# Kernel optimization log

Measured on AMD Instinct MI355X. Metric: run time of the kernel, lower is better.

The kernel has to match this reference:

```python
import jax, jax.numpy as jnp
import numpy as np

B, S, H = 4, 1024, 1024
R = 512          # num_rules
M = 1024         # memory_size
HEADS = 16
STEPS = 3        # inference_steps
TEMP = 1.0       # softmax_temperature
LN_EPS = 1e-5


def setup_inputs() -> dict:
    key = jax.random.key(0)
    ks = jax.random.split(key, 40)
    std = 0.02
    p = lambda k, shp: (jax.random.normal(k, shp, jnp.float32) * std)
    inp = {
        "hidden_states": jax.random.normal(ks[0], (B, S, H), jnp.float32),
        "rule_embeddings": p(ks[1], (R, H)),
        "rule_sel_w": p(ks[2], (H, R)), "rule_sel_b": jnp.zeros((R,), jnp.float32),
        # self-attention (nn.MultiheadAttention) projections
        "attn_wq": p(ks[3], (H, H)), "attn_bq": jnp.zeros((H,), jnp.float32),
        "attn_wk": p(ks[4], (H, H)), "attn_bk": jnp.zeros((H,), jnp.float32),
        "attn_wv": p(ks[5], (H, H)), "attn_bv": jnp.zeros((H,), jnp.float32),
        "attn_wo": p(ks[6], (H, H)), "attn_bo": jnp.zeros((H,), jnp.float32),
        # memory bank + key/query/value projections
        "memory": p(ks[7], (M, H)),
        "mem_q_w": p(ks[8], (H, H)), "mem_q_b": jnp.zeros((H,), jnp.float32),
        "mem_k_w": p(ks[9], (H, H)), "mem_k_b": jnp.zeros((H,), jnp.float32),
        "mem_v_w": p(ks[10], (H, H)), "mem_v_b": jnp.zeros((H,), jnp.float32),
        # memory_attention (nn.MultiheadAttention) projections
        "mattn_wq": p(ks[11], (H, H)), "mattn_bq": jnp.zeros((H,), jnp.float32),
        "mattn_wk": p(ks[12], (H, H)), "mattn_bk": jnp.zeros((H,), jnp.float32),
        "mattn_wv": p(ks[13], (H, H)), "mattn_bv": jnp.zeros((H,), jnp.float32),
        "mattn_wo": p(ks[14], (H, H)), "mattn_bo": jnp.zeros((H,), jnp.float32),
        # rule_application: Linear(2H,H)+LN+GELU+Linear(H,H)
        "ra_w1": p(ks[15], (2 * H, H)), "ra_b1": jnp.zeros((H,), jnp.float32),
        "ra_ln_s": jnp.ones((H,), jnp.float32), "ra_ln_b": jnp.zeros((H,), jnp.float32),
        "ra_w2": p(ks[16], (H, H)), "ra_b2": jnp.zeros((H,), jnp.float32),
        # confidence_scorer
        "conf_w": p(ks[17], (H, 1)), "conf_b": jnp.zeros((1,), jnp.float32),
    }
    return inp


def _mha(q_in, k_in, v_in, wq, bq, wk, bk, wv, bv, wo, bo):
    # standard nn.MultiheadAttention math (batch_first, eval mode -> no dropout)
    b, sq, h = q_in.shape
    d = h // HEADS
    qh = (q_in @ wq + bq).reshape(b, sq, HEADS, d)
    kh = (k_in @ wk + bk).reshape(b, -1, HEADS, d)
    vh = (v_in @ wv + bv).reshape(b, -1, HEADS, d)
    scores = jnp.einsum('bqhd,bkhd->bhqk', qh, kh) / jnp.sqrt(jnp.asarray(d, qh.dtype))
    probs = jax.nn.softmax(scores, axis=-1)
    out = jnp.einsum('bhqk,bkhd->bqhd', probs, vh).reshape(b, sq, h)
    return out @ wo + bo


def _ln(x, s, b):
    mu = x.mean(-1, keepdims=True)
    var = ((x - mu) ** 2).mean(-1, keepdims=True)
    return (x - mu) / jnp.sqrt(var + LN_EPS) * s + b


def reference(hidden_states, rule_embeddings, rule_sel_w, rule_sel_b,
              attn_wq, attn_bq, attn_wk, attn_bk, attn_wv, attn_bv, attn_wo, attn_bo,
              memory, mem_q_w, mem_q_b, mem_k_w, mem_k_b, mem_v_w, mem_v_b,
              mattn_wq, mattn_bq, mattn_wk, mattn_bk, mattn_wv, mattn_bv, mattn_wo, mattn_bo,
              ra_w1, ra_b1, ra_ln_s, ra_ln_b, ra_w2, ra_b2, conf_w, conf_b):
    h = hidden_states
    b = h.shape[0]
    # memory keys/values are input-independent: project once, broadcast over batch
    mk = jnp.broadcast_to((memory @ mem_k_w + mem_k_b)[None], (b, M, H))
    mv = jnp.broadcast_to((memory @ mem_v_w + mem_v_b)[None], (b, M, H))
    for _ in range(STEPS):
        # rule routing: soft selection over the rule-embedding table
        rule_probs = jax.nn.softmax((h @ rule_sel_w + rule_sel_b) / TEMP, axis=-1)  # [B,S,R]
        selected = jnp.einsum('bsr,rh->bsh', rule_probs, rule_embeddings)           # [B,S,H]
        # self-attention reasoning
        h = h + _mha(h, h, h, attn_wq, attn_bq, attn_wk, attn_bk,
                     attn_wv, attn_bv, attn_wo, attn_bo)
        # memory attention
        mq = h @ mem_q_w + mem_q_b
        h = h + _mha(mq, mk, mv, mattn_wq, mattn_bq, mattn_wk, mattn_bk,
                     mattn_wv, mattn_bv, mattn_wo, mattn_bo)
        # rule application MLP on [h ; selected_rules]
        x = jnp.concatenate([h, selected], axis=-1)                                  # [B,S,2H]
        u = jax.nn.gelu(_ln(x @ ra_w1 + ra_b1, ra_ln_s, ra_ln_b), approximate=False)
        h = h + (u @ ra_w2 + ra_b2)
    confidence = jax.nn.sigmoid(h @ conf_w + conf_b)  # [B,S,1]
    return h, confidence
```

## Files before the change

kernel.cpp:

```cpp
#include <hip/hip_runtime.h>
#include <stdint.h>

typedef _Float16 f16;
typedef __attribute__((ext_vector_type(4))) float floatx4;
typedef __attribute__((ext_vector_type(8))) f16   f16x8;
typedef __attribute__((ext_vector_type(4))) f16   f16x4;

#define GLD_LDS16(gp, lp)                                                                      \
  __builtin_amdgcn_global_load_lds((const __attribute__((address_space(1))) void*)(uintptr_t)(gp), \
                                   (__attribute__((address_space(3))) void*)(uintptr_t)(lp), 16, 0, 0)

struct SrlOut {
  int n0;
  const float* bias;
  const float* resid;
  float* Cf; f16* Cb;
  int ldcf, ldcb, transV;
  long long sCb, sCh;
};
struct SrlGemmArgs {
  const f16* A; const f16* B;
  int M, N, K, lda, ldb;
  long long sAb, sAh, sBb, sBh;
  float alpha;
  int nOuts;
  SrlOut out[4];
};

template<int BN>
__global__ __launch_bounds__(256, 2) void srl_gemm(SrlGemmArgs g) {
  constexpr int BM = 128, BK = 64;
  constexpr int BCH = BN / 32;
  constexpr int MI  = (BN == 128) ? 4 : 2;
  __shared__ f16 As[2][BM * BK];
  __shared__ f16 Bs[2][BN * BK];
  const int tid  = threadIdx.x;
  const int wid  = tid >> 6;
  const int lane = tid & 63;
  const int z  = blockIdx.z, zh = z & 15, zb = z >> 4;

  const int gx = gridDim.x;
  const int NT = gx * gridDim.y;
  const int L  = blockIdx.y * gx + blockIdx.x;
  const int W  = ((NT & 7) == 0) ? ((L & 7) * (NT >> 3) + (L >> 3)) : L;
  const int tn = (W % gx) * BN;
  const int tm = (W / gx) * BM;

  const f16* Ab = g.A + (long long)zb * g.sAb + (long long)zh * g.sAh + (long long)tm * g.lda;
  const f16* Bb = g.B + (long long)zb * g.sBb + (long long)zh * g.sBh + (long long)tn * g.ldb;
  const int maxAr = g.M - 1 - tm;
  const int maxBr = g.N - 1 - tn;

  int aR[4], aO[4];
#pragma unroll
  for (int i = 0; i < 4; ++i) {
    int e = wid * 2048 + i * 512 + lane * 8;
    int r = e >> 6, s = (e >> 3) & 7;
    aR[i] = r; aO[i] = ((s - r) & 7) * 8;
  }
  int bR[BCH], bO[BCH];
#pragma unroll
  for (int i = 0; i < BCH; ++i) {
    int e = wid * (BN * 16) + i * 512 + lane * 8;
    int r = e >> 6, s = (e >> 3) & 7;
    bR[i] = r; bO[i] = ((s - r) & 7) * 8;
  }

  f16x8 pa[4], pb[BCH];
  auto loadT = [&](int k0) {
#pragma unroll
    for (int i = 0; i < 4; ++i) {
      int r = aR[i] <= maxAr ? aR[i] : maxAr;
      pa[i] = *(const f16x8*)(Ab + (long long)r * g.lda + (k0 + aO[i]));
    }
#pragma unroll
    for (int i = 0; i < BCH; ++i) {
      int r = bR[i] <= maxBr ? bR[i] : maxBr;
      pb[i] = *(const f16x8*)(Bb + (long long)r * g.ldb + (k0 + bO[i]));
    }
  };
  auto storeT = [&](int buf) {
    f16* a = As[buf] + wid * 2048 + lane * 8;
    f16* b = Bs[buf] + wid * (BN * 16) + lane * 8;
#pragma unroll
    for (int i = 0; i < 4; ++i) *(f16x8*)(a + i * 512) = pa[i];
#pragma unroll
    for (int i = 0; i < BCH; ++i) *(f16x8*)(b + i * 512) = pb[i];
  };

  floatx4 acc[MI][4];
#pragma unroll
  for (int a = 0; a < MI; ++a)
#pragma unroll
    for (int b = 0; b < 4; ++b) {
      acc[a][b][0] = 0.f; acc[a][b][1] = 0.f; acc[a][b][2] = 0.f; acc[a][b][3] = 0.f;
    }

  const int wm = (BN == 128) ? (wid & 1) * 64 : wid * 32;
  const int wn = (BN == 128) ? (wid >> 1) * 64 : 0;
  const int lm = lane & 15;
  const int quad = lane >> 4;

  const int T = g.K / BK;
  loadT(0);
  storeT(0);
  if (T > 1) loadT(BK);
  __syncthreads();

  for (int t = 0; t < T; ++t) {
    const int cb = t & 1;
    if (t + 1 < T) {
      storeT(cb ^ 1);
      if (t + 2 < T) loadT((t + 2) * BK);
    }
#pragma unroll
    for (int ks = 0; ks < 2; ++ks) {
      f16x8 af[MI], bfr[4];
#pragma unroll
      for (int mi = 0; mi < MI; ++mi) {
        int row = wm + mi * 16 + lm;
        int sg = ((ks * 4 + quad) + row) & 7;
        af[mi] = *(const f16x8*)(As[cb] + row * 64 + sg * 8);
      }
#pragma unroll
      for (int ni = 0; ni < 4; ++ni) {
        int row = wn + ni * 16 + lm;
        int sg = ((ks * 4 + quad) + row) & 7;
        bfr[ni] = *(const f16x8*)(Bs[cb] + row * 64 + sg * 8);
      }
#pragma unroll
      for (int mi = 0; mi < MI; ++mi)
#pragma unroll
        for (int ni = 0; ni < 4; ++ni)
          acc[mi][ni] = __builtin_amdgcn_mfma_f32_16x16x32_f16(af[mi], bfr[ni], acc[mi][ni], 0, 0, 0);
    }
    __syncthreads();
  }

  int oi = 0;
  for (int j = 1; j < g.nOuts; ++j)
    if (tn >= g.out[j].n0) oi = j;
  const SrlOut O = g.out[oi];
  const long long zc = (long long)zb * O.sCb + (long long)zh * O.sCh;
#pragma unroll
  for (int mi = 0; mi < MI; ++mi) {
#pragma unroll
    for (int r = 0; r < 4; ++r) {
      int m = tm + wm + mi * 16 + quad * 4 + r;
      if (m >= g.M) continue;
#pragma unroll
      for (int ni = 0; ni < 4; ++ni) {
        int n = tn + wn + ni * 16 + lm;
        if (n >= g.N) continue;
        int nl = n - O.n0;
        float v = acc[mi][ni][r] * g.alpha;
        if (O.bias)  v += O.bias[nl];
        if (O.resid) v += O.resid[(long long)m * O.ldcf + nl];
        if (O.Cf)    O.Cf[zc + (long long)m * O.ldcf + nl] = v;
        if (O.Cb) {
          long long idx = O.transV
              ? ((long long)(m >> 10) * 1048576 + (long long)nl * 1024 + (m & 1023))
              : (zc + (long long)m * O.ldcb + nl);
          O.Cb[idx] = (f16)v;
        }
      }
    }
  }
}

struct SrlFlashArgs {
  const f16* Q; const f16* K; const f16* VT; f16* O;
  long long sQb, sKb, sVb;
  float scale;
};

__global__ __launch_bounds__(256, 2) void srl_flash(SrlFlashArgs a) {
  __shared__ f16 Qs[8192];
  __shared__ f16 Ks[8192];
  __shared__ f16 VTs[8192];
  __shared__ f16 Ps[4][4096];
  const int tid = threadIdx.x, wid = tid >> 6, lane = tid & 63;
  const int quad = lane >> 4, c = lane & 15;
  const int L = blockIdx.x;
  const int bh = (L & 7) + ((L >> 6) << 3);
  const int qt = (L >> 3) & 7;
  const int b = bh >> 4, h = bh & 15;
  const f16* Qg = a.Q + (long long)b * a.sQb + (long long)qt * 131072 + h * 64;
  const f16* Kg = a.K + (long long)b * a.sKb + h * 64;
  const f16* Vg = a.VT + (long long)b * a.sVb + (long long)h * 65536;
  f16* Og = a.O + (long long)b * 1048576 + (long long)qt * 131072 + h * 64;

  int rRow[4], rOff[4];
#pragma unroll
  for (int i = 0; i < 4; ++i) {
    int e = wid * 2048 + i * 512 + lane * 8;
    int r = e >> 6, gL = (e >> 3) & 7;
    rRow[i] = r; rOff[i] = ((gL - r) & 7) * 8;
  }
  int vRow[4], vOff[4];
#pragma unroll
  for (int i = 0; i < 4; ++i) {
    int e = wid * 2048 + i * 512 + lane * 8;
    int d = e >> 7, gL = (e >> 3) & 15;
    vRow[i] = d; vOff[i] = ((gL - (d & 7)) & 15) * 8;
  }

#pragma unroll
  for (int i = 0; i < 4; ++i)
    GLD_LDS16(Qg + (long long)rRow[i] * 1024 + rOff[i], Qs + wid * 2048 + i * 512);
  __syncthreads();

  const int wq = wid * 32;
  f16x8 qf[2][2];
#pragma unroll
  for (int nf = 0; nf < 2; ++nf)
#pragma unroll
    for (int ch = 0; ch < 2; ++ch) {
      int row = wq + nf * 16 + c;
      int slot = ((ch * 4 + quad) + row) & 7;
      f16x8 v = *(const f16x8*)(Qs + row * 64 + slot * 8);
      f16 sc = (f16)a.scale;
#pragma unroll
      for (int j = 0; j < 8; ++j) v[j] = v[j] * sc;
      qf[nf][ch] = v;
    }

  float l_s[2] = {0.f, 0.f};
  floatx4 Oa[2][4];
#pragma unroll
  for (int nf = 0; nf < 2; ++nf)
#pragma unroll
    for (int no = 0; no < 4; ++no) {
      Oa[nf][no][0] = 0.f; Oa[nf][no][1] = 0.f; Oa[nf][no][2] = 0.f; Oa[nf][no][3] = 0.f;
    }

  for (int t = 0; t < 8; ++t) {
    __syncthreads();
#pragma unroll
    for (int i = 0; i < 4; ++i)
      GLD_LDS16(Kg + (long long)(t * 128 + rRow[i]) * 1024 + rOff[i], Ks + wid * 2048 + i * 512);
#pragma unroll
    for (int i = 0; i < 4; ++i)
      GLD_LDS16(Vg + (long long)vRow[i] * 1024 + (t * 128 + vOff[i]), VTs + wid * 2048 + i * 512);
    __syncthreads();

    floatx4 sT[2][8];
#pragma unroll
    for (int nf = 0; nf < 2; ++nf)
#pragma unroll
      for (int mf = 0; mf < 8; ++mf) {
        sT[nf][mf][0] = 0.f; sT[nf][mf][1] = 0.f; sT[nf][mf][2] = 0.f; sT[nf][mf][3] = 0.f;
      }
#pragma unroll
    for (int ch = 0; ch < 2; ++ch)
#pragma unroll
      for (int mf = 0; mf < 8; ++mf) {
        int key = mf * 16 + c;
        int slot = ((ch * 4 + quad) + key) & 7;
        f16x8 kf = *(const f16x8*)(Ks + key * 64 + slot * 8);
        sT[0][mf] = __builtin_amdgcn_mfma_f32_16x16x32_f16(kf, qf[0][ch], sT[0][mf], 0, 0, 0);
        sT[1][mf] = __builtin_amdgcn_mfma_f32_16x16x32_f16(kf, qf[1][ch], sT[1][mf], 0, 0, 0);
      }

#pragma unroll
    for (int nf = 0; nf < 2; ++nf) {
      float lt = 0.f;
      const int q = nf * 16 + c;
#pragma unroll
      for (int mf = 0; mf < 8; ++mf) {
        f16x4 pk;
#pragma unroll
        for (int r = 0; r < 4; ++r) {
          float p = __builtin_amdgcn_exp2f(sT[nf][mf][r]);
          lt += p;
          pk[r] = (f16)p;
        }
        int kg = mf * 2 + (quad >> 1), sub = (quad & 1) * 4;
        int slot = (kg + (q & 7)) & 15;
        *(f16x4*)(Ps[wid] + q * 128 + slot * 8 + sub) = pk;
      }
      lt += __shfl_xor(lt, 16);
      lt += __shfl_xor(lt, 32);
      l_s[nf] += lt;
    }
#pragma unroll
    for (int cc = 0; cc < 4; ++cc) {
      f16x8 af[2];
#pragma unroll
      for (int nf = 0; nf < 2; ++nf) {
        int q = nf * 16 + c;
        int slot = ((cc * 4 + quad) + (q & 7)) & 15;
        af[nf] = *(const f16x8*)(Ps[wid] + q * 128 + slot * 8);
      }
#pragma unroll
      for (int no = 0; no < 4; ++no) {
        int d = no * 16 + c;
        int slot = ((cc * 4 + quad) + (d & 7)) & 15;
        f16x8 vf = *(const f16x8*)(VTs + d * 128 + slot * 8);
        Oa[0][no] = __builtin_amdgcn_mfma_f32_16x16x32_f16(af[0], vf, Oa[0][no], 0, 0, 0);
        Oa[1][no] = __builtin_amdgcn_mfma_f32_16x16x32_f16(af[1], vf, Oa[1][no], 0, 0, 0);
      }
    }
  }

#pragma unroll
  for (int nf = 0; nf < 2; ++nf)
#pragma unroll
    for (int r = 0; r < 4; ++r) {
      float li = 1.f / __shfl(l_s[nf], quad * 4 + r);
      int qrow = wq + nf * 16 + quad * 4 + r;
#pragma unroll
      for (int no = 0; no < 4; ++no)
        Qs[qrow * 64 + no * 16 + c] = (f16)(Oa[nf][no][r] * li);
    }
  __syncthreads();
#pragma unroll
  for (int i = 0; i < 4; ++i) {
    int e = wid * 2048 + i * 512 + lane * 8;
    int row = e >> 6, col = e & 63;
    *(f16x8*)(Og + (long long)row * 1024 + col) = *(const f16x8*)(Qs + e);
  }
}

__global__ __launch_bounds__(256) void srl_softmax_rule(const float* logits, f16* probs) {
  __shared__ float red[16];
  const long long row = blockIdx.x;
  const float* p = logits + row * 512;
  const int tid = threadIdx.x;
  float v0 = p[tid], v1 = p[tid + 256];
  float mx = fmaxf(v0, v1);
#pragma unroll
  for (int o = 32; o > 0; o >>= 1) mx = fmaxf(mx, __shfl_down(mx, o));
  const int wid = tid >> 6, lane = tid & 63;
  if (lane == 0) red[wid] = mx;
  __syncthreads();
  if (tid == 0) red[8] = fmaxf(fmaxf(red[0], red[1]), fmaxf(red[2], red[3]));
  __syncthreads();
  mx = red[8];
  float e0 = __expf(v0 - mx), e1 = __expf(v1 - mx);
  float s = e0 + e1;
#pragma unroll
  for (int o = 32; o > 0; o >>= 1) s += __shfl_down(s, o);
  if (lane == 0) red[wid + 4] = s;
  __syncthreads();
  if (tid == 0) red[9] = 1.f / (red[4] + red[5] + red[6] + red[7]);
  __syncthreads();
  const float inv = red[9];
  probs[row * 512 + tid] = (f16)(e0 * inv);
  probs[row * 512 + tid + 256] = (f16)(e1 * inv);
}

__global__ __launch_bounds__(256) void srl_ln_gelu(const float* x, const float* gam, const float* bet, f16* out) {
  __shared__ float red[16];
  const long long row = blockIdx.x;
  const float* p = x + row * 1024;
  const int tid = threadIdx.x;
  float4 xv = *(const float4*)(p + tid * 4);
  float v[4] = {xv.x, xv.y, xv.z, xv.w};
  float s = v[0] + v[1] + v[2] + v[3];
  float s2 = v[0] * v[0] + v[1] * v[1] + v[2] * v[2] + v[3] * v[3];
#pragma unroll
  for (int o = 32; o > 0; o >>= 1) { s += __shfl_down(s, o); s2 += __shfl_down(s2, o); }
  const int wid = tid >> 6, lane = tid & 63;
  if (lane == 0) { red[wid] = s; red[wid + 4] = s2; }
  __syncthreads();
  if (tid == 0) {
    float ts = red[0] + red[1] + red[2] + red[3];
    float ts2 = red[4] + red[5] + red[6] + red[7];
    float mu = ts * (1.f / 1024.f);
    float var = ts2 * (1.f / 1024.f) - mu * mu;
    red[8] = mu;
    red[9] = rsqrtf(var + 1e-5f);
  }
  __syncthreads();
  const float mu = red[8], rstd = red[9];
  f16x4 o4;
#pragma unroll
  for (int i = 0; i < 4; ++i) {
    int c = tid * 4 + i;
    float t = (v[i] - mu) * rstd * gam[c] + bet[c];
    float ge = 0.5f * t * (1.f + erff(t * 0.70710678118654752f));
    o4[i] = (f16)ge;
  }
  *(f16x4*)(out + row * 1024 + tid * 4) = o4;
}

struct SrlTcEnt { const float* src; f16* dst; int rows, cols, trans, tileStart; };
struct SrlTcArgs { SrlTcEnt e[16]; };

__global__ __launch_bounds__(256) void srl_convert_weights(SrlTcArgs a) {
  __shared__ float t[32][33];
  const int bt = blockIdx.x;
  int ei = 0;
#pragma unroll
  for (int j = 1; j < 16; ++j)
    if (bt >= a.e[j].tileStart) ei = j;
  SrlTcEnt E = a.e[ei];
  const int lt = bt - E.tileStart;
  const int tcols = E.cols >> 5;
  const int tr = lt / tcols;
  const int tc = lt - tr * tcols;
  const int r = threadIdx.x >> 5;
  const int c = threadIdx.x & 31;
  if (!E.trans) {
#pragma unroll
    for (int p = 0; p < 4; ++p) {
      long long rr = tr * 32 + r + p * 8;
      long long idx = rr * E.cols + tc * 32 + c;
      E.dst[idx] = (f16)E.src[idx];
    }
  } else {
#pragma unroll
    for (int p = 0; p < 4; ++p)
      t[r + p * 8][c] = E.src[(long long)(tr * 32 + r + p * 8) * E.cols + tc * 32 + c];
    __syncthreads();
#pragma unroll
    for (int p = 0; p < 4; ++p)
      E.dst[(long long)(tc * 32 + r + p * 8) * E.rows + tr * 32 + c] = (f16)t[c][r + p * 8];
  }
}

__global__ __launch_bounds__(256) void srl_prep_bias(const float* rsel_b, const float* bq,
                                                     const float* bk, const float* bv,
                                                     const float* bmq, const float* maq_w,
                                                     const float* bmaq,
                                                     float* bias_qkvr, float* bcomp) {
  int i = blockIdx.x * 256 + threadIdx.x;
  if (i < 3584) {
    float v;
    if (i < 512) v = rsel_b[i];
    else if (i < 1536) v = bq[i - 512];
    else if (i < 2560) v = bk[i - 1536];
    else v = bv[i - 2560];
    bias_qkvr[i] = v;
  } else if (i < 3584 + 1024) {
    int m = i - 3584;
    float s = bmaq[m];
    for (int t = 0; t < 1024; ++t) s += bmq[t] * maq_w[(long long)t * 1024 + m];
    bcomp[m] = s;
  }
}

__global__ __launch_bounds__(256) void srl_h_init(const float* hidden, float* hf, f16* hx) {
  long long base = ((long long)blockIdx.x * 256 + threadIdx.x) * 4;
  float4 v = *(const float4*)(hidden + base);
  *(float4*)(hf + base) = v;
  long long row = base >> 10;
  int col = (int)(base & 1023);
  f16x4 b;
  b[0] = (f16)v.x; b[1] = (f16)v.y; b[2] = (f16)v.z; b[3] = (f16)v.w;
  *(f16x4*)(hx + row * 2048 + col) = b;
}

__global__ __launch_bounds__(256) void srl_finalize(const float* hf, const float* w, const float* b,
                                                    float* out, float* conf) {
  const int bid = blockIdx.x;
  if (bid < 4096) {
    long long base = ((long long)bid * 256 + threadIdx.x) * 4;
    *(float4*)(out + base) = *(const float4*)(hf + base);
  } else {
    const int row = (bid - 4096) * 4 + (threadIdx.x >> 6);
    const int lane = threadIdx.x & 63;
    const float* p = hf + (long long)row * 1024;
    float s = 0.f;
    for (int j = lane; j < 1024; j += 64) s += p[j] * w[j];
#pragma unroll
    for (int o = 32; o > 0; o >>= 1) s += __shfl_down(s, o);
    if (lane == 0) conf[row] = 1.f / (1.f + __expf(-(s + b[0])));
  }
}

extern "C" void kernel_launch(void* const* d_in, const int* in_sizes, int n_in,
                              void* d_out, int out_size, void* d_ws, size_t ws_size,
                              hipStream_t stream) {
  (void)in_sizes; (void)n_in; (void)out_size; (void)ws_size;
  const float* in_hidden   = (const float*)d_in[0];
  const float* in_rule_emb = (const float*)d_in[1];
  const float* in_rsel_w   = (const float*)d_in[2];
  const float* in_rsel_b   = (const float*)d_in[3];
  const float* in_attn_wq  = (const float*)d_in[4];
  const float* in_attn_bq  = (const float*)d_in[5];
  const float* in_attn_wk  = (const float*)d_in[6];
  const float* in_attn_bk  = (const float*)d_in[7];
  const float* in_attn_wv  = (const float*)d_in[8];
  const float* in_attn_bv  = (const float*)d_in[9];
  const float* in_attn_wo  = (const float*)d_in[10];
  const float* in_attn_bo  = (const float*)d_in[11];
  const float* in_memory   = (const float*)d_in[12];
  const float* in_mq_w     = (const float*)d_in[13];
  const float* in_mq_b     = (const float*)d_in[14];
  const float* in_mk_w     = (const float*)d_in[15];
  const float* in_mk_b     = (const float*)d_in[16];
  const float* in_mv_w     = (const float*)d_in[17];
  const float* in_mv_b     = (const float*)d_in[18];
  const float* in_maq_w    = (const float*)d_in[19];
  const float* in_maq_b    = (const float*)d_in[20];
  const float* in_mak_w    = (const float*)d_in[21];
  const float* in_mak_b    = (const float*)d_in[22];
  const float* in_mav_w    = (const float*)d_in[23];
  const float* in_mav_b    = (const float*)d_in[24];
  const float* in_mao_w    = (const float*)d_in[25];
  const float* in_mao_b    = (const float*)d_in[26];
  const float* in_ra_w1    = (const float*)d_in[27];
  const float* in_ra_b1    = (const float*)d_in[28];
  const float* in_ln_s     = (const float*)d_in[29];
  const float* in_ln_b     = (const float*)d_in[30];
  const float* in_ra_w2    = (const float*)d_in[31];
  const float* in_ra_b2    = (const float*)d_in[32];
  const float* in_conf_w   = (const float*)d_in[33];
  const float* in_conf_b   = (const float*)d_in[34];

  char* ws = (char*)d_ws;
  size_t off = 0;
  auto alloc = [&](size_t bytes) -> void* {
    void* p = ws + off;
    off = (off + bytes + 255) & ~(size_t)255;
    return p;
  };
  f16* wt_qkvr    = (f16*)alloc(3584 * 1024 * 2);
  float* bias_qkvr= (float*)alloc(3584 * 4);
  f16* wt_attn_o  = (f16*)alloc(1048576 * 2);
  f16* wt_mq_comp = (f16*)alloc(1048576 * 2);
  float* bcomp    = (float*)alloc(1024 * 4);
  f16* wt_mattn_o = (f16*)alloc(1048576 * 2);
  f16* wt_ra1     = (f16*)alloc(2097152 * 2);
  f16* wt_ra2     = (f16*)alloc(1048576 * 2);
  f16* wt_remb    = (f16*)alloc(524288 * 2);
  f16* wt_mem_kv  = (f16*)alloc(2097152 * 2);
  f16* wt_mattn_k = (f16*)alloc(1048576 * 2);
  f16* wt_mattn_v = (f16*)alloc(1048576 * 2);
  f16* mem_h      = (f16*)alloc(1048576 * 2);
  f16* mk_h       = (f16*)alloc(1048576 * 2);
  f16* mv_h       = (f16*)alloc(1048576 * 2);
  f16* mak_h      = (f16*)alloc(1048576 * 2);
  f16* mavT_h     = (f16*)alloc(1048576 * 2);
  float* h_f      = (float*)alloc(4194304 * 4);
  f16* hx         = (f16*)alloc(8388608 * 2);
  f16* q_h        = (f16*)alloc(4194304 * 2);
  f16* k_h        = (f16*)alloc(4194304 * 2);
  f16* vT_h       = (f16*)alloc(4194304 * 2);
  f16* ctx_h      = (f16*)alloc(4194304 * 2);
  f16* u_h        = (f16*)alloc(4194304 * 2);
  char* arena     = (char*)alloc(16777216);
  float* logits_f = (float*)arena;
  f16* probs_h    = (f16*)(arena + 8388608);
  float* ra1_f    = (float*)arena;
  f16* mqw_nt     = (f16*)arena;
  f16* wmaq_t     = (f16*)(arena + 2097152);

  auto mkOut = [](int n0, const float* bias, const float* resid, float* Cf, int ldcf,
                  f16* Cb, int ldcb, int transV, long long sCb, long long sCh) {
    SrlOut o;
    o.n0 = n0; o.bias = bias; o.resid = resid; o.Cf = Cf; o.Cb = Cb;
    o.ldcf = ldcf; o.ldcb = ldcb; o.transV = transV; o.sCb = sCb; o.sCh = sCh;
    return o;
  };
  auto run = [&](int BN, int M, int N, int K, const f16* A, int lda, const f16* B, int ldb,
                 float alpha, int Z, long long sAb, long long sAh, long long sBb, long long sBh,
                 SrlGemmArgs g) {
    g.A = A; g.B = B; g.M = M; g.N = N; g.K = K; g.lda = lda; g.ldb = ldb;
    g.sAb = sAb; g.sAh = sAh; g.sBb = sBb; g.sBh = sBh; g.alpha = alpha;
    dim3 grid((N + BN - 1) / BN, (M + 127) / 128, Z);
    if (BN == 128) hipLaunchKernelGGL(srl_gemm<128>, grid, dim3(256), 0, stream, g);
    else           hipLaunchKernelGGL(srl_gemm<64>,  grid, dim3(256), 0, stream, g);
  };
  auto run1 = [&](int BN, int M, int N, int K, const f16* A, int lda, const f16* B, int ldb,
                  float alpha, const float* bias, const float* resid, float* Cf, int ldcf,
                  f16* Cb, int ldcb, int transV) {
    SrlGemmArgs g{};
    g.nOuts = 1;
    g.out[0] = mkOut(0, bias, resid, Cf, ldcf, Cb, ldcb, transV, 0, 0);
    run(BN, M, N, K, A, lda, B, ldb, alpha, 1, 0, 0, 0, 0, g);
  };

  SrlTcArgs tc;
  int ts = 0;
  auto setent = [&](int i, const float* s, f16* d, int rows, int cols, int trans) {
    tc.e[i].src = s; tc.e[i].dst = d; tc.e[i].rows = rows; tc.e[i].cols = cols;
    tc.e[i].trans = trans; tc.e[i].tileStart = ts;
    ts += (rows / 32) * (cols / 32);
  };
  setent(0,  in_attn_wq, wt_qkvr + 512 * 1024, 1024, 1024, 1);
  setent(1,  in_attn_wk, wt_qkvr + 1536 * 1024, 1024, 1024, 1);
  setent(2,  in_attn_wv, wt_qkvr + 2560 * 1024, 1024, 1024, 1);
  setent(3,  in_rsel_w,  wt_qkvr, 1024, 512, 1);
  setent(4,  in_attn_wo, wt_attn_o, 1024, 1024, 1);
  setent(5,  in_mq_w,    mqw_nt, 1024, 1024, 0);
  setent(6,  in_maq_w,   wmaq_t, 1024, 1024, 1);
  setent(7,  in_mak_w,   wt_mattn_k, 1024, 1024, 1);
  setent(8,  in_mav_w,   wt_mattn_v, 1024, 1024, 1);
  setent(9,  in_mk_w,    wt_mem_kv, 1024, 1024, 1);
  setent(10, in_mv_w,    wt_mem_kv + 1048576, 1024, 1024, 1);
  setent(11, in_mao_w,   wt_mattn_o, 1024, 1024, 1);
  setent(12, in_ra_w1,   wt_ra1, 2048, 1024, 1);
  setent(13, in_ra_w2,   wt_ra2, 1024, 1024, 1);
  setent(14, in_rule_emb, wt_remb, 512, 1024, 1);
  setent(15, in_memory,  mem_h, 1024, 1024, 0);
  hipLaunchKernelGGL(srl_convert_weights, dim3(ts), dim3(256), 0, stream, tc);
  hipLaunchKernelGGL(srl_prep_bias, dim3(18), dim3(256), 0, stream,
                     in_rsel_b, in_attn_bq, in_attn_bk, in_attn_bv,
                     in_mq_b, in_maq_w, in_maq_b, bias_qkvr, bcomp);
  hipLaunchKernelGGL(srl_h_init, dim3(4096), dim3(256), 0, stream, in_hidden, h_f, hx);

  {
    SrlGemmArgs g{};
    g.nOuts = 2;
    g.out[0] = mkOut(0, in_mk_b, nullptr, nullptr, 0, mk_h, 1024, 0, 0, 0);
    g.out[1] = mkOut(1024, in_mv_b, nullptr, nullptr, 0, mv_h, 1024, 0, 0, 0);
    run(64, 1024, 2048, 1024, mem_h, 1024, wt_mem_kv, 1024, 1.f, 1, 0, 0, 0, 0, g);
  }
  run1(64, 1024, 1024, 1024, mk_h, 1024, wt_mattn_k, 1024, 1.f, in_mak_b, nullptr, nullptr, 0, mak_h, 1024, 0);
  run1(64, 1024, 1024, 1024, mv_h, 1024, wt_mattn_v, 1024, 1.f, in_mav_b, nullptr, nullptr, 0, mavT_h, 0, 1);
  run1(64, 1024, 1024, 1024, wmaq_t, 1024, mqw_nt, 1024, 1.f, nullptr, nullptr, nullptr, 0, wt_mq_comp, 1024, 0);

  const float kLog2e = 1.4426950408889634f;
  for (int step = 0; step < 3; ++step) {
    {
      SrlGemmArgs g{};
      g.nOuts = 4;
      g.out[0] = mkOut(0,    bias_qkvr,        nullptr, logits_f, 512, nullptr, 0, 0, 0, 0);
      g.out[1] = mkOut(512,  bias_qkvr + 512,  nullptr, nullptr, 0, q_h, 1024, 0, 0, 0);
      g.out[2] = mkOut(1536, bias_qkvr + 1536, nullptr, nullptr, 0, k_h, 1024, 0, 0, 0);
      g.out[3] = mkOut(2560, bias_qkvr + 2560, nullptr, nullptr, 0, vT_h, 0, 1, 0, 0);
      run(128, 4096, 3584, 1024, hx, 2048, wt_qkvr, 1024, 1.f, 1, 0, 0, 0, 0, g);
    }
    hipLaunchKernelGGL(srl_softmax_rule, dim3(4096), dim3(256), 0, stream, logits_f, probs_h);
    run1(64, 4096, 1024, 512, probs_h, 512, wt_remb, 512, 1.f, nullptr, nullptr, nullptr, 0, hx + 1024, 2048, 0);
    {
      SrlFlashArgs fa;
      fa.Q = q_h; fa.K = k_h; fa.VT = vT_h; fa.O = ctx_h;
      fa.sQb = 1048576; fa.sKb = 1048576; fa.sVb = 1048576; fa.scale = 0.125f * kLog2e;
      hipLaunchKernelGGL(srl_flash, dim3(512), dim3(256), 0, stream, fa);
    }
    run1(64, 4096, 1024, 1024, ctx_h, 1024, wt_attn_o, 1024, 1.f, in_attn_bo, h_f, h_f, 1024, hx, 2048, 0);
    run1(64, 4096, 1024, 1024, hx, 2048, wt_mq_comp, 1024, 1.f, bcomp, nullptr, nullptr, 0, k_h, 1024, 0);
    {
      SrlFlashArgs fa;
      fa.Q = k_h; fa.K = mak_h; fa.VT = mavT_h; fa.O = ctx_h;
      fa.sQb = 1048576; fa.sKb = 0; fa.sVb = 0; fa.scale = 0.125f * kLog2e;
      hipLaunchKernelGGL(srl_flash, dim3(512), dim3(256), 0, stream, fa);
    }
    run1(64, 4096, 1024, 1024, ctx_h, 1024, wt_mattn_o, 1024, 1.f, in_mao_b, h_f, h_f, 1024, hx, 2048, 0);
    run1(64, 4096, 1024, 2048, hx, 2048, wt_ra1, 2048, 1.f, in_ra_b1, nullptr, ra1_f, 1024, nullptr, 0, 0);
    hipLaunchKernelGGL(srl_ln_gelu, dim3(4096), dim3(256), 0, stream, ra1_f, in_ln_s, in_ln_b, u_h);
    run1(64, 4096, 1024, 1024, u_h, 1024, wt_ra2, 1024, 1.f, in_ra_b2, h_f, h_f, 1024, hx, 2048, 0);
  }

  hipLaunchKernelGGL(srl_finalize, dim3(5120), dim3(256), 0, stream, h_f, in_conf_w, in_conf_b,
                     (float*)d_out, (float*)d_out + 4194304);
}
```

Measured before the change: 1.241 ms.

## Add single-buffer 128x64 direct-to-LDS GEMM for QKVR and split-K the ra1 GEMM

Adds srl_gemm2, a 2-wave 128x64 tile kernel that loads A and B straight into LDS through global_load_lds with a single buffer. The fused QKV+rule GEMM now uses it in place of the 128x128 register-staged kernel. The K=2048 rule-application GEMM is split into two K=1024 halves via the z grid dimension, each writing its own fp32 partial. The LayerNorm+GELU kernel then sums both partials and the bias. The aim is more blocks in flight for better occupancy, at the cost of an extra 16MB fp32 partial write and read, and a single LDS buffer with no prefetch in the new kernel.

```diff
diff --git a/kernel.cpp b/kernel.cpp
--- a/kernel.cpp
+++ b/kernel.cpp
@@ -27,11 +27,8 @@
   SrlOut out[4];
 };
 
-template<int BN>
-__global__ __launch_bounds__(256, 2) void srl_gemm(SrlGemmArgs g) {
-  constexpr int BM = 128, BK = 64;
-  constexpr int BCH = BN / 32;
-  constexpr int MI  = (BN == 128) ? 4 : 2;
+__global__ __launch_bounds__(256, 2) void srl_gemm_db(SrlGemmArgs g) {
+  constexpr int BN = 64, BM = 128, BK = 64, BCH = 2, MI = 2;
   __shared__ f16 As[2][BM * BK];
   __shared__ f16 Bs[2][BN * BK];
   const int tid  = threadIdx.x;
@@ -96,8 +93,7 @@
       acc[a][b][0] = 0.f; acc[a][b][1] = 0.f; acc[a][b][2] = 0.f; acc[a][b][3] = 0.f;
     }
 
-  const int wm = (BN == 128) ? (wid & 1) * 64 : wid * 32;
-  const int wn = (BN == 128) ? (wid >> 1) * 64 : 0;
+  const int wm = wid * 32;
   const int lm = lane & 15;
   const int quad = lane >> 4;
 
@@ -124,7 +120,7 @@
       }
 #pragma unroll
       for (int ni = 0; ni < 4; ++ni) {
-        int row = wn + ni * 16 + lm;
+        int row = ni * 16 + lm;
         int sg = ((ks * 4 + quad) + row) & 7;
         bfr[ni] = *(const f16x8*)(Bs[cb] + row * 64 + sg * 8);
       }
@@ -150,7 +146,124 @@
       if (m >= g.M) continue;
 #pragma unroll
       for (int ni = 0; ni < 4; ++ni) {
-        int n = tn + wn + ni * 16 + lm;
+        int n = tn + ni * 16 + lm;
+        if (n >= g.N) continue;
+        int nl = n - O.n0;
+        float v = acc[mi][ni][r] * g.alpha;
+        if (O.bias)  v += O.bias[nl];
+        if (O.resid) v += O.resid[(long long)m * O.ldcf + nl];
+        if (O.Cf)    O.Cf[zc + (long long)m * O.ldcf + nl] = v;
+        if (O.Cb) {
+          long long idx = O.transV
+              ? ((long long)(m >> 10) * 1048576 + (long long)nl * 1024 + (m & 1023))
+              : (zc + (long long)m * O.ldcb + nl);
+          O.Cb[idx] = (f16)v;
+        }
+      }
+    }
+  }
+}
+
+__global__ __launch_bounds__(128, 2) void srl_gemm2(SrlGemmArgs g) {
+  constexpr int BK = 64;
+  __shared__ f16 As[128 * BK];
+  __shared__ f16 Bs[64 * BK];
+  const int tid  = threadIdx.x;
+  const int wid  = tid >> 6;
+  const int lane = tid & 63;
+  const int z  = blockIdx.z, zh = z & 15, zb = z >> 4;
+
+  const int gx = gridDim.x;
+  const int NT = gx * gridDim.y;
+  const int L  = blockIdx.y * gx + blockIdx.x;
+  const int W  = ((NT & 7) == 0) ? ((L & 7) * (NT >> 3) + (L >> 3)) : L;
+  const int tn = (W % gx) * 64;
+  const int tm = (W / gx) * 128;
+
+  const f16* Ab = g.A + (long long)zb * g.sAb + (long long)zh * g.sAh + (long long)tm * g.lda;
+  const f16* Bb = g.B + (long long)zb * g.sBb + (long long)zh * g.sBh + (long long)tn * g.ldb;
+  const int maxAr = g.M - 1 - tm;
+  const int maxBr = g.N - 1 - tn;
+
+  int aR[8], aO[8];
+#pragma unroll
+  for (int i = 0; i < 8; ++i) {
+    int e = wid * 4096 + i * 512 + lane * 8;
+    int r = e >> 6, s = (e >> 3) & 7;
+    aR[i] = r; aO[i] = ((s - r) & 7) * 8;
+  }
+  int bR[4], bO[4];
+#pragma unroll
+  for (int i = 0; i < 4; ++i) {
+    int e = wid * 2048 + i * 512 + lane * 8;
+    int r = e >> 6, s = (e >> 3) & 7;
+    bR[i] = r; bO[i] = ((s - r) & 7) * 8;
+  }
+  f16* lA = As + wid * 4096;
+  f16* lB = Bs + wid * 2048;
+
+  floatx4 acc[4][4];
+#pragma unroll
+  for (int a = 0; a < 4; ++a)
+#pragma unroll
+    for (int b = 0; b < 4; ++b) {
+      acc[a][b][0] = 0.f; acc[a][b][1] = 0.f; acc[a][b][2] = 0.f; acc[a][b][3] = 0.f;
+    }
+
+  const int wm = wid * 64;
+  const int lm = lane & 15;
+  const int quad = lane >> 4;
+
+  for (int k0 = 0; k0 < g.K; k0 += BK) {
+    __syncthreads();
+#pragma unroll
+    for (int i = 0; i < 8; ++i) {
+      int r = aR[i] <= maxAr ? aR[i] : maxAr;
+      GLD_LDS16(Ab + (long long)r * g.lda + (k0 + aO[i]), lA + i * 512);
+    }
+#pragma unroll
+    for (int i = 0; i < 4; ++i) {
+      int r = bR[i] <= maxBr ? bR[i] : maxBr;
+      GLD_LDS16(Bb + (long long)r * g.ldb + (k0 + bO[i]), lB + i * 512);
+    }
+    __syncthreads();
+#pragma unroll
+    for (int ks = 0; ks < 2; ++ks) {
+      f16x8 af[4], bfr[4];
+#pragma unroll
+      for (int mi = 0; mi < 4; ++mi) {
+        int row = wm + mi * 16 + lm;
+        int sg = ((ks * 4 + quad) + row) & 7;
+        af[mi] = *(const f16x8*)(As + row * 64 + sg * 8);
+      }
+#pragma unroll
+      for (int ni = 0; ni < 4; ++ni) {
+        int row = ni * 16 + lm;
+        int sg = ((ks * 4 + quad) + row) & 7;
+        bfr[ni] = *(const f16x8*)(Bs + row * 64 + sg * 8);
+      }
+#pragma unroll
+      for (int mi = 0; mi < 4; ++mi)
+#pragma unroll
+        for (int ni = 0; ni < 4; ++ni)
+          acc[mi][ni] = __builtin_amdgcn_mfma_f32_16x16x32_f16(af[mi], bfr[ni], acc[mi][ni], 0, 0, 0);
+    }
+  }
+
+  int oi = 0;
+  for (int j = 1; j < g.nOuts; ++j)
+    if (tn >= g.out[j].n0) oi = j;
+  const SrlOut O = g.out[oi];
+  const long long zc = (long long)zb * O.sCb + (long long)zh * O.sCh;
+#pragma unroll
+  for (int mi = 0; mi < 4; ++mi) {
+#pragma unroll
+    for (int r = 0; r < 4; ++r) {
+      int m = tm + wm + mi * 16 + quad * 4 + r;
+      if (m >= g.M) continue;
+#pragma unroll
+      for (int ni = 0; ni < 4; ++ni) {
+        int n = tn + ni * 16 + lm;
         if (n >= g.N) continue;
         int nl = n - O.n0;
         float v = acc[mi][ni][r] * g.alpha;
@@ -350,13 +463,16 @@
   probs[row * 512 + tid + 256] = (f16)(e1 * inv);
 }
 
-__global__ __launch_bounds__(256) void srl_ln_gelu(const float* x, const float* gam, const float* bet, f16* out) {
+__global__ __launch_bounds__(256) void srl_ln_gelu2(const float* x0, const float* x1,
+                                                    const float* b1,
+                                                    const float* gam, const float* bet, f16* out) {
   __shared__ float red[16];
   const long long row = blockIdx.x;
-  const float* p = x + row * 1024;
   const int tid = threadIdx.x;
-  float4 xv = *(const float4*)(p + tid * 4);
-  float v[4] = {xv.x, xv.y, xv.z, xv.w};
+  float4 a0 = *(const float4*)(x0 + row * 1024 + tid * 4);
+  float4 a1 = *(const float4*)(x1 + row * 1024 + tid * 4);
+  float4 bb = *(const float4*)(b1 + tid * 4);
+  float v[4] = {a0.x + a1.x + bb.x, a0.y + a1.y + bb.y, a0.z + a1.z + bb.z, a0.w + a1.w + bb.w};
   float s = v[0] + v[1] + v[2] + v[3];
   float s2 = v[0] * v[0] + v[1] * v[1] + v[2] * v[2] + v[3] * v[3];
 #pragma unroll
@@ -541,10 +657,11 @@
   f16* vT_h       = (f16*)alloc(4194304 * 2);
   f16* ctx_h      = (f16*)alloc(4194304 * 2);
   f16* u_h        = (f16*)alloc(4194304 * 2);
-  char* arena     = (char*)alloc(16777216);
+  char* arena     = (char*)alloc(33554432);
   float* logits_f = (float*)arena;
   f16* probs_h    = (f16*)(arena + 8388608);
-  float* ra1_f    = (float*)arena;
+  float* ra1_p0   = (float*)arena;
+  float* ra1_p1   = (float*)(arena + 16777216);
   f16* mqw_nt     = (f16*)arena;
   f16* wmaq_t     = (f16*)(arena + 2097152);
 
@@ -555,22 +672,28 @@
     o.ldcf = ldcf; o.ldcb = ldcb; o.transV = transV; o.sCb = sCb; o.sCh = sCh;
     return o;
   };
-  auto run = [&](int BN, int M, int N, int K, const f16* A, int lda, const f16* B, int ldb,
-                 float alpha, int Z, long long sAb, long long sAh, long long sBb, long long sBh,
-                 SrlGemmArgs g) {
+  auto runDb = [&](int M, int N, int K, const f16* A, int lda, const f16* B, int ldb,
+                   float alpha, int Z, long long sAb, long long sAh, long long sBb, long long sBh,
+                   SrlGemmArgs g) {
     g.A = A; g.B = B; g.M = M; g.N = N; g.K = K; g.lda = lda; g.ldb = ldb;
     g.sAb = sAb; g.sAh = sAh; g.sBb = sBb; g.sBh = sBh; g.alpha = alpha;
-    dim3 grid((N + BN - 1) / BN, (M + 127) / 128, Z);
-    if (BN == 128) hipLaunchKernelGGL(srl_gemm<128>, grid, dim3(256), 0, stream, g);
-    else           hipLaunchKernelGGL(srl_gemm<64>,  grid, dim3(256), 0, stream, g);
+    dim3 grid((N + 63) / 64, (M + 127) / 128, Z);
+    hipLaunchKernelGGL(srl_gemm_db, grid, dim3(256), 0, stream, g);
   };
-  auto run1 = [&](int BN, int M, int N, int K, const f16* A, int lda, const f16* B, int ldb,
-                  float alpha, const float* bias, const float* resid, float* Cf, int ldcf,
-                  f16* Cb, int ldcb, int transV) {
+  auto runDb1 = [&](int M, int N, int K, const f16* A, int lda, const f16* B, int ldb,
+                    float alpha, const float* bias, const float* resid, float* Cf, int ldcf,
+                    f16* Cb, int ldcb, int transV) {
     SrlGemmArgs g{};
     g.nOuts = 1;
     g.out[0] = mkOut(0, bias, resid, Cf, ldcf, Cb, ldcb, transV, 0, 0);
-    run(BN, M, N, K, A, lda, B, ldb, alpha, 1, 0, 0, 0, 0, g);
+    runDb(M, N, K, A, lda, B, ldb, alpha, 1, 0, 0, 0, 0, g);
+  };
+  auto runW2 = [&](int M, int N, int K, const f16* A, int lda, const f16* B, int ldb,
+                   float alpha, SrlGemmArgs g) {
+    g.A = A; g.B = B; g.M = M; g.N = N; g.K = K; g.lda = lda; g.ldb = ldb;
+    g.sAb = 0; g.sAh = 0; g.sBb = 0; g.sBh = 0; g.alpha = alpha;
+    dim3 grid((N + 63) / 64, (M + 127) / 128, 1);
+    hipLaunchKernelGGL(srl_gemm2, grid, dim3(128), 0, stream, g);
   };
 
   SrlTcArgs tc;
@@ -607,11 +730,11 @@
     g.nOuts = 2;
     g.out[0] = mkOut(0, in_mk_b, nullptr, nullptr, 0, mk_h, 1024, 0, 0, 0);
     g.out[1] = mkOut(1024, in_mv_b, nullptr, nullptr, 0, mv_h, 1024, 0, 0, 0);
-    run(64, 1024, 2048, 1024, mem_h, 1024, wt_mem_kv, 1024, 1.f, 1, 0, 0, 0, 0, g);
-  }
-  run1(64, 1024, 1024, 1024, mk_h, 1024, wt_mattn_k, 1024, 1.f, in_mak_b, nullptr, nullptr, 0, mak_h, 1024, 0);
-  run1(64, 1024, 1024, 1024, mv_h, 1024, wt_mattn_v, 1024, 1.f, in_mav_b, nullptr, nullptr, 0, mavT_h, 0, 1);
-  run1(64, 1024, 1024, 1024, wmaq_t, 1024, mqw_nt, 1024, 1.f, nullptr, nullptr, nullptr, 0, wt_mq_comp, 1024, 0);
+    runDb(1024, 2048, 1024, mem_h, 1024, wt_mem_kv, 1024, 1.f, 1, 0, 0, 0, 0, g);
+  }
+  runDb1(1024, 1024, 1024, mk_h, 1024, wt_mattn_k, 1024, 1.f, in_mak_b, nullptr, nullptr, 0, mak_h, 1024, 0);
+  runDb1(1024, 1024, 1024, mv_h, 1024, wt_mattn_v, 1024, 1.f, in_mav_b, nullptr, nullptr, 0, mavT_h, 0, 1);
+  runDb1(1024, 1024, 1024, wmaq_t, 1024, mqw_nt, 1024, 1.f, nullptr, nullptr, nullptr, 0, wt_mq_comp, 1024, 0);
 
   const float kLog2e = 1.4426950408889634f;
   for (int step = 0; step < 3; ++step) {
@@ -622,28 +745,34 @@
       g.out[1] = mkOut(512,  bias_qkvr + 512,  nullptr, nullptr, 0, q_h, 1024, 0, 0, 0);
       g.out[2] = mkOut(1536, bias_qkvr + 1536, nullptr, nullptr, 0, k_h, 1024, 0, 0, 0);
       g.out[3] = mkOut(2560, bias_qkvr + 2560, nullptr, nullptr, 0, vT_h, 0, 1, 0, 0);
-      run(128, 4096, 3584, 1024, hx, 2048, wt_qkvr, 1024, 1.f, 1, 0, 0, 0, 0, g);
+      runW2(4096, 3584, 1024, hx, 2048, wt_qkvr, 1024, 1.f, g);
     }
     hipLaunchKernelGGL(srl_softmax_rule, dim3(4096), dim3(256), 0, stream, logits_f, probs_h);
-    run1(64, 4096, 1024, 512, probs_h, 512, wt_remb, 512, 1.f, nullptr, nullptr, nullptr, 0, hx + 1024, 2048, 0);
+    runDb1(4096, 1024, 512, probs_h, 512, wt_remb, 512, 1.f, nullptr, nullptr, nullptr, 0, hx + 1024, 2048, 0);
     {
       SrlFlashArgs fa;
       fa.Q = q_h; fa.K = k_h; fa.VT = vT_h; fa.O = ctx_h;
       fa.sQb = 1048576; fa.sKb = 1048576; fa.sVb = 1048576; fa.scale = 0.125f * kLog2e;
       hipLaunchKernelGGL(srl_flash, dim3(512), dim3(256), 0, stream, fa);
     }
-    run1(64, 4096, 1024, 1024, ctx_h, 1024, wt_attn_o, 1024, 1.f, in_attn_bo, h_f, h_f, 1024, hx, 2048, 0);
-    run1(64, 4096, 1024, 1024, hx, 2048, wt_mq_comp, 1024, 1.f, bcomp, nullptr, nullptr, 0, k_h, 1024, 0);
+    runDb1(4096, 1024, 1024, ctx_h, 1024, wt_attn_o, 1024, 1.f, in_attn_bo, h_f, h_f, 1024, hx, 2048, 0);
+    runDb1(4096, 1024, 1024, hx, 2048, wt_mq_comp, 1024, 1.f, bcomp, nullptr, nullptr, 0, k_h, 1024, 0);
     {
       SrlFlashArgs fa;
       fa.Q = k_h; fa.K = mak_h; fa.VT = mavT_h; fa.O = ctx_h;
       fa.sQb = 1048576; fa.sKb = 0; fa.sVb = 0; fa.scale = 0.125f * kLog2e;
       hipLaunchKernelGGL(srl_flash, dim3(512), dim3(256), 0, stream, fa);
     }
-    run1(64, 4096, 1024, 1024, ctx_h, 1024, wt_mattn_o, 1024, 1.f, in_mao_b, h_f, h_f, 1024, hx, 2048, 0);
-    run1(64, 4096, 1024, 2048, hx, 2048, wt_ra1, 2048, 1.f, in_ra_b1, nullptr, ra1_f, 1024, nullptr, 0, 0);
-    hipLaunchKernelGGL(srl_ln_gelu, dim3(4096), dim3(256), 0, stream, ra1_f, in_ln_s, in_ln_b, u_h);
-    run1(64, 4096, 1024, 1024, u_h, 1024, wt_ra2, 1024, 1.f, in_ra_b2, h_f, h_f, 1024, hx, 2048, 0);
+    runDb1(4096, 1024, 1024, ctx_h, 1024, wt_mattn_o, 1024, 1.f, in_mao_b, h_f, h_f, 1024, hx, 2048, 0);
+    {
+      SrlGemmArgs g{};
+      g.nOuts = 1;
+      g.out[0] = mkOut(0, nullptr, nullptr, ra1_p0, 1024, nullptr, 0, 0, 0, 4194304);
+      runDb(4096, 1024, 1024, hx, 2048, wt_ra1, 2048, 1.f, 2, 0, 1024, 0, 1024, g);
+    }
+    hipLaunchKernelGGL(srl_ln_gelu2, dim3(4096), dim3(256), 0, stream, ra1_p0, ra1_p1,
+                       in_ra_b1, in_ln_s, in_ln_b, u_h);
+    runDb1(4096, 1024, 1024, u_h, 1024, wt_ra2, 1024, 1.f, in_ra_b2, h_f, h_f, 1024, hx, 2048, 0);
   }
 
   hipLaunchKernelGGL(srl_finalize, dim3(5120), dim3(256), 0, stream, h_f, in_conf_w, in_conf_b,
```

After: 1.294 ms. +4.2%, slower.

## Load GEMM tiles straight into LDS and use 64x64 tiles with higher occupancy

Applied to the files above, without the earlier changes.

The GEMM kernel drops its register-staged double-buffered LDS pipeline. It now issues global_load_lds instructions that write each K-slice directly into a single LDS buffer, with a barrier before and after each load. The kernel is templated on BM/BN/min-waves: the large QKV-plus-rule GEMM keeps 128x128 tiles, and every other GEMM switches to 64x64 tiles with a launch bound that asks for more resident blocks. The aim is to cut VGPR staging traffic and register pressure so more waves can hide latency. In exchange, explicit load/compute overlap within a block is lost and the smaller tiles reuse each loaded operand less.

```diff
diff --git a/kernel.cpp b/kernel.cpp
--- a/kernel.cpp
+++ b/kernel.cpp
@@ -27,13 +27,15 @@
   SrlOut out[4];
 };
 
-template<int BN>
-__global__ __launch_bounds__(256, 2) void srl_gemm(SrlGemmArgs g) {
-  constexpr int BM = 128, BK = 64;
+template<int BM, int BN, int MINW>
+__global__ __launch_bounds__(256, MINW) void srl_gemm(SrlGemmArgs g) {
+  constexpr int BK = 64;
+  constexpr int ACH = BM / 32;
   constexpr int BCH = BN / 32;
-  constexpr int MI  = (BN == 128) ? 4 : 2;
-  __shared__ f16 As[2][BM * BK];
-  __shared__ f16 Bs[2][BN * BK];
+  constexpr int MI  = (BM == 128 && BN == 128) ? 4 : 2;
+  constexpr int NI  = (BN == 128) ? 4 : ((BM == 128) ? 4 : 2);
+  __shared__ f16 As[BM * BK];
+  __shared__ f16 Bs[BN * BK];
   const int tid  = threadIdx.x;
   const int wid  = tid >> 6;
   const int lane = tid & 63;
@@ -51,10 +53,10 @@
   const int maxAr = g.M - 1 - tm;
   const int maxBr = g.N - 1 - tn;
 
-  int aR[4], aO[4];
-#pragma unroll
-  for (int i = 0; i < 4; ++i) {
-    int e = wid * 2048 + i * 512 + lane * 8;
+  int aR[ACH], aO[ACH];
+#pragma unroll
+  for (int i = 0; i < ACH; ++i) {
+    int e = wid * (BM * 16) + i * 512 + lane * 8;
     int r = e >> 6, s = (e >> 3) & 7;
     aR[i] = r; aO[i] = ((s - r) & 7) * 8;
   }
@@ -65,76 +67,61 @@
     int r = e >> 6, s = (e >> 3) & 7;
     bR[i] = r; bO[i] = ((s - r) & 7) * 8;
   }
-
-  f16x8 pa[4], pb[BCH];
-  auto loadT = [&](int k0) {
-#pragma unroll
-    for (int i = 0; i < 4; ++i) {
+  f16* lA = As + wid * (BM * 16);
+  f16* lB = Bs + wid * (BN * 16);
+
+  floatx4 acc[MI][NI];
+#pragma unroll
+  for (int a = 0; a < MI; ++a)
+#pragma unroll
+    for (int b = 0; b < NI; ++b) {
+      acc[a][b][0] = 0.f; acc[a][b][1] = 0.f; acc[a][b][2] = 0.f; acc[a][b][3] = 0.f;
+    }
+
+  const int wm = (BM == 128 && BN == 128) ? (wid & 1) * 64
+               : (BN == 128)              ? 0
+               : (BM == 128)              ? wid * 32
+                                          : (wid & 1) * 32;
+  const int wn = (BM == 128 && BN == 128) ? (wid >> 1) * 64
+               : (BM == 64 && BN == 64)   ? (wid >> 1) * 32
+                                          : 0;
+  const int lm = lane & 15;
+  const int quad = lane >> 4;
+
+  for (int k0 = 0; k0 < g.K; k0 += BK) {
+    __syncthreads();
+#pragma unroll
+    for (int i = 0; i < ACH; ++i) {
       int r = aR[i] <= maxAr ? aR[i] : maxAr;
-      pa[i] = *(const f16x8*)(Ab + (long long)r * g.lda + (k0 + aO[i]));
+      GLD_LDS16(Ab + (long long)r * g.lda + (k0 + aO[i]), lA + i * 512);
     }
 #pragma unroll
     for (int i = 0; i < BCH; ++i) {
       int r = bR[i] <= maxBr ? bR[i] : maxBr;
-      pb[i] = *(const f16x8*)(Bb + (long long)r * g.ldb + (k0 + bO[i]));
-    }
-  };
-  auto storeT = [&](int buf) {
-    f16* a = As[buf] + wid * 2048 + lane * 8;
-    f16* b = Bs[buf] + wid * (BN * 16) + lane * 8;
-#pragma unroll
-    for (int i = 0; i < 4; ++i) *(f16x8*)(a + i * 512) = pa[i];
-#pragma unroll
-    for (int i = 0; i < BCH; ++i) *(f16x8*)(b + i * 512) = pb[i];
-  };
-
-  floatx4 acc[MI][4];
-#pragma unroll
-  for (int a = 0; a < MI; ++a)
-#pragma unroll
-    for (int b = 0; b < 4; ++b) {
-      acc[a][b][0] = 0.f; acc[a][b][1] = 0.f; acc[a][b][2] = 0.f; acc[a][b][3] = 0.f;
-    }
-
-  const int wm = (BN == 128) ? (wid & 1) * 64 : wid * 32;
-  const int wn = (BN == 128) ? (wid >> 1) * 64 : 0;
-  const int lm = lane & 15;
-  const int quad = lane >> 4;
-
-  const int T = g.K / BK;
-  loadT(0);
-  storeT(0);
-  if (T > 1) loadT(BK);
-  __syncthreads();
-
-  for (int t = 0; t < T; ++t) {
-    const int cb = t & 1;
-    if (t + 1 < T) {
-      storeT(cb ^ 1);
-      if (t + 2 < T) loadT((t + 2) * BK);
-    }
+      GLD_LDS16(Bb + (long long)r * g.ldb + (k0 + bO[i]), lB + i * 512);
+    }
+    __syncthreads();
 #pragma unroll
     for (int ks = 0; ks < 2; ++ks) {
-      f16x8 af[MI], bfr[4];
+      f16x8 af[MI], bfr[NI];
 #pragma unroll
       for (int mi = 0; mi < MI; ++mi) {
         int row = wm + mi * 16 + lm;
         int sg = ((ks * 4 + quad) + row) & 7;
-        af[mi] = *(const f16x8*)(As[cb] + row * 64 + sg * 8);
-      }
-#pragma unroll
-      for (int ni = 0; ni < 4; ++ni) {
+        af[mi] = *(const f16x8*)(As + row * 64 + sg * 8);
+      }
+#pragma unroll
+      for (int ni = 0; ni < NI; ++ni) {
         int row = wn + ni * 16 + lm;
         int sg = ((ks * 4 + quad) + row) & 7;
-        bfr[ni] = *(const f16x8*)(Bs[cb] + row * 64 + sg * 8);
+        bfr[ni] = *(const f16x8*)(Bs + row * 64 + sg * 8);
       }
 #pragma unroll
       for (int mi = 0; mi < MI; ++mi)
 #pragma unroll
-        for (int ni = 0; ni < 4; ++ni)
+        for (int ni = 0; ni < NI; ++ni)
           acc[mi][ni] = __builtin_amdgcn_mfma_f32_16x16x32_f16(af[mi], bfr[ni], acc[mi][ni], 0, 0, 0);
     }
-    __syncthreads();
   }
 
   int oi = 0;
@@ -149,7 +136,7 @@
       int m = tm + wm + mi * 16 + quad * 4 + r;
       if (m >= g.M) continue;
 #pragma unroll
-      for (int ni = 0; ni < 4; ++ni) {
+      for (int ni = 0; ni < NI; ++ni) {
         int n = tn + wn + ni * 16 + lm;
         if (n >= g.N) continue;
         int nl = n - O.n0;
@@ -555,22 +542,30 @@
     o.ldcf = ldcf; o.ldcb = ldcb; o.transV = transV; o.sCb = sCb; o.sCh = sCh;
     return o;
   };
-  auto run = [&](int BN, int M, int N, int K, const f16* A, int lda, const f16* B, int ldb,
-                 float alpha, int Z, long long sAb, long long sAh, long long sBb, long long sBh,
-                 SrlGemmArgs g) {
+  auto runBig = [&](int M, int N, int K, const f16* A, int lda, const f16* B, int ldb,
+                    float alpha, SrlGemmArgs g) {
     g.A = A; g.B = B; g.M = M; g.N = N; g.K = K; g.lda = lda; g.ldb = ldb;
-    g.sAb = sAb; g.sAh = sAh; g.sBb = sBb; g.sBh = sBh; g.alpha = alpha;
-    dim3 grid((N + BN - 1) / BN, (M + 127) / 128, Z);
-    if (BN == 128) hipLaunchKernelGGL(srl_gemm<128>, grid, dim3(256), 0, stream, g);
-    else           hipLaunchKernelGGL(srl_gemm<64>,  grid, dim3(256), 0, stream, g);
+    g.sAb = 0; g.sAh = 0; g.sBb = 0; g.sBh = 0; g.alpha = alpha;
+    dim3 grid((N + 127) / 128, (M + 127) / 128, 1);
+    hipLaunchKernelGGL((srl_gemm<128, 128, 2>), grid, dim3(256), 0, stream, g);
   };
-  auto run1 = [&](int BN, int M, int N, int K, const f16* A, int lda, const f16* B, int ldb,
-                  float alpha, const float* bias, const float* resid, float* Cf, int ldcf,
-                  f16* Cb, int ldcb, int transV) {
+  auto runSm1 = [&](int M, int N, int K, const f16* A, int lda, const f16* B, int ldb,
+                    float alpha, const float* bias, const float* resid, float* Cf, int ldcf,
+                    f16* Cb, int ldcb, int transV) {
     SrlGemmArgs g{};
     g.nOuts = 1;
     g.out[0] = mkOut(0, bias, resid, Cf, ldcf, Cb, ldcb, transV, 0, 0);
-    run(BN, M, N, K, A, lda, B, ldb, alpha, 1, 0, 0, 0, 0, g);
+    g.A = A; g.B = B; g.M = M; g.N = N; g.K = K; g.lda = lda; g.ldb = ldb;
+    g.sAb = 0; g.sAh = 0; g.sBb = 0; g.sBh = 0; g.alpha = alpha;
+    dim3 grid((N + 63) / 64, (M + 63) / 64, 1);
+    hipLaunchKernelGGL((srl_gemm<64, 64, 4>), grid, dim3(256), 0, stream, g);
+  };
+  auto runSm = [&](int M, int N, int K, const f16* A, int lda, const f16* B, int ldb,
+                   float alpha, SrlGemmArgs g) {
+    g.A = A; g.B = B; g.M = M; g.N = N; g.K = K; g.lda = lda; g.ldb = ldb;
+    g.sAb = 0; g.sAh = 0; g.sBb = 0; g.sBh = 0; g.alpha = alpha;
+    dim3 grid((N + 63) / 64, (M + 63) / 64, 1);
+    hipLaunchKernelGGL((srl_gemm<64, 64, 4>), grid, dim3(256), 0, stream, g);
   };
 
   SrlTcArgs tc;
@@ -607,11 +602,11 @@
     g.nOuts = 2;
     g.out[0] = mkOut(0, in_mk_b, nullptr, nullptr, 0, mk_h, 1024, 0, 0, 0);
     g.out[1] = mkOut(1024, in_mv_b, nullptr, nullptr, 0, mv_h, 1024, 0, 0, 0);
-    run(64, 1024, 2048, 1024, mem_h, 1024, wt_mem_kv, 1024, 1.f, 1, 0, 0, 0, 0, g);
-  }
-  run1(64, 1024, 1024, 1024, mk_h, 1024, wt_mattn_k, 1024, 1.f, in_mak_b, nullptr, nullptr, 0, mak_h, 1024, 0);
-  run1(64, 1024, 1024, 1024, mv_h, 1024, wt_mattn_v, 1024, 1.f, in_mav_b, nullptr, nullptr, 0, mavT_h, 0, 1);
-  run1(64, 1024, 1024, 1024, wmaq_t, 1024, mqw_nt, 1024, 1.f, nullptr, nullptr, nullptr, 0, wt_mq_comp, 1024, 0);
+    runSm(1024, 2048, 1024, mem_h, 1024, wt_mem_kv, 1024, 1.f, g);
+  }
+  runSm1(1024, 1024, 1024, mk_h, 1024, wt_mattn_k, 1024, 1.f, in_mak_b, nullptr, nullptr, 0, mak_h, 1024, 0);
+  runSm1(1024, 1024, 1024, mv_h, 1024, wt_mattn_v, 1024, 1.f, in_mav_b, nullptr, nullptr, 0, mavT_h, 0, 1);
+  runSm1(1024, 1024, 1024, wmaq_t, 1024, mqw_nt, 1024, 1.f, nullptr, nullptr, nullptr, 0, wt_mq_comp, 1024, 0);
 
   const float kLog2e = 1.4426950408889634f;
   for (int step = 0; step < 3; ++step) {
@@ -622,28 +617,28 @@
       g.out[1] = mkOut(512,  bias_qkvr + 512,  nullptr, nullptr, 0, q_h, 1024, 0, 0, 0);
       g.out[2] = mkOut(1536, bias_qkvr + 1536, nullptr, nullptr, 0, k_h, 1024, 0, 0, 0);
       g.out[3] = mkOut(2560, bias_qkvr + 2560, nullptr, nullptr, 0, vT_h, 0, 1, 0, 0);
-      run(128, 4096, 3584, 1024, hx, 2048, wt_qkvr, 1024, 1.f, 1, 0, 0, 0, 0, g);
+      runBig(4096, 3584, 1024, hx, 2048, wt_qkvr, 1024, 1.f, g);
     }
     hipLaunchKernelGGL(srl_softmax_rule, dim3(4096), dim3(256), 0, stream, logits_f, probs_h);
-    run1(64, 4096, 1024, 512, probs_h, 512, wt_remb, 512, 1.f, nullptr, nullptr, nullptr, 0, hx + 1024, 2048, 0);
+    runSm1(4096, 1024, 512, probs_h, 512, wt_remb, 512, 1.f, nullptr, nullptr, nullptr, 0, hx + 1024, 2048, 0);
     {
       SrlFlashArgs fa;
       fa.Q = q_h; fa.K = k_h; fa.VT = vT_h; fa.O = ctx_h;
       fa.sQb = 1048576; fa.sKb = 1048576; fa.sVb = 1048576; fa.scale = 0.125f * kLog2e;
       hipLaunchKernelGGL(srl_flash, dim3(512), dim3(256), 0, stream, fa);
     }
-    run1(64, 4096, 1024, 1024, ctx_h, 1024, wt_attn_o, 1024, 1.f, in_attn_bo, h_f, h_f, 1024, hx, 2048, 0);
-    run1(64, 4096, 1024, 1024, hx, 2048, wt_mq_comp, 1024, 1.f, bcomp, nullptr, nullptr, 0, k_h, 1024, 0);
+    runSm1(4096, 1024, 1024, ctx_h, 1024, wt_attn_o, 1024, 1.f, in_attn_bo, h_f, h_f, 1024, hx, 2048, 0);
+    runSm1(4096, 1024, 1024, hx, 2048, wt_mq_comp, 1024, 1.f, bcomp, nullptr, nullptr, 0, k_h, 1024, 0);
     {
       SrlFlashArgs fa;
       fa.Q = k_h; fa.K = mak_h; fa.VT = mavT_h; fa.O = ctx_h;
       fa.sQb = 1048576; fa.sKb = 0; fa.sVb = 0; fa.scale = 0.125f * kLog2e;
       hipLaunchKernelGGL(srl_flash, dim3(512), dim3(256), 0, stream, fa);
     }
-    run1(64, 4096, 1024, 1024, ctx_h, 1024, wt_mattn_o, 1024, 1.f, in_mao_b, h_f, h_f, 1024, hx, 2048, 0);
-    run1(64, 4096, 1024, 2048, hx, 2048, wt_ra1, 2048, 1.f, in_ra_b1, nullptr, ra1_f, 1024, nullptr, 0, 0);
+    runSm1(4096, 1024, 1024, ctx_h, 1024, wt_mattn_o, 1024, 1.f, in_mao_b, h_f, h_f, 1024, hx, 2048, 0);
+    runSm1(4096, 1024, 2048, hx, 2048, wt_ra1, 2048, 1.f, in_ra_b1, nullptr, ra1_f, 1024, nullptr, 0, 0);
     hipLaunchKernelGGL(srl_ln_gelu, dim3(4096), dim3(256), 0, stream, ra1_f, in_ln_s, in_ln_b, u_h);
-    run1(64, 4096, 1024, 1024, u_h, 1024, wt_ra2, 1024, 1.f, in_ra_b2, h_f, h_f, 1024, hx, 2048, 0);
+    runSm1(4096, 1024, 1024, u_h, 1024, wt_ra2, 1024, 1.f, in_ra_b2, h_f, h_f, 1024, hx, 2048, 0);
   }
 
   hipLaunchKernelGGL(srl_finalize, dim3(5120), dim3(256), 0, stream, h_f, in_conf_w, in_conf_b,
```

Result: faster. 1.149 ms (-7.4%).
